# Kernel tuning notes

Hardware: AMD Instinct MI355X
Metric: run time of the kernel (lower is better)

Reference implementation:

```python
import jax, jax.numpy as jnp
import numpy as np

B, N_PER = 1048576, 32
MAX_COUNT = 5  # counts >= 5 lumped into the '>4' bucket (severity 3)


def setup_inputs() -> dict:
    key = jax.random.key(0)
    k1, k2, k3 = jax.random.split(key, 3)
    x1 = jax.random.uniform(k1, (B, N_PER), dtype=jnp.float32)
    x2 = jax.random.uniform(k2, (B, N_PER), dtype=jnp.float32)
    x3 = jax.random.uniform(k3, (B, N_PER), dtype=jnp.float32)
    return {"x1": x1, "x2": x2, "x3": x3}


def _count_distribution(p):
    # p: [B, N] independent fact probabilities.
    # Poisson-binomial DP over facts with count capped at MAX_COUNT (absorbing).
    b = p.shape[0]
    init = jnp.zeros((b, MAX_COUNT + 1), p.dtype).at[:, 0].set(1.0)

    def step(c, pi):
        pi = pi[:, None]                              # [B,1]
        shifted = jnp.pad(c[:, :-1], ((0, 0), (1, 0)))  # count+1
        new = c * (1.0 - pi) + shifted * pi
        # absorbing top bucket: staying in >=MAX_COUNT regardless of pi
        new = new.at[:, -1].add(c[:, -1] * pi[:, 0])
        return new, None

    counts, _ = jax.lax.scan(step, init, p.T)  # scan over facts axis
    return counts  # [B, MAX_COUNT+1]


def reference(x1, x2, x3):
    p = jnp.concatenate([x1, x2, x3], axis=1)  # [B, 96]
    c = _count_distribution(p)
    # severity(0): n==0; severity(1): 1<=n<=2; severity(2): 3<=n<=4;
    # severity(3): n>4; severity(4): never derivable -> 0
    sev = jnp.stack(
        [c[:, 0], c[:, 1] + c[:, 2], c[:, 3] + c[:, 4], c[:, 5],
         jnp.zeros_like(c[:, 0])],
        axis=1,
    )
    return sev  # [B, 5]
```

## Files before the change

kernel.cpp:

```cpp
#include <hip/hip_runtime.h>


#define THREADS 256

__global__ __launch_bounds__(THREADS, 6) void hemorrhage_kernel(
    const float* __restrict__ x1,
    const float* __restrict__ x2,
    const float* __restrict__ x3,
    float* __restrict__ out)
{
    const int t = threadIdx.x;
    const int m = t & 7;
    const int row = blockIdx.x * (THREADS / 8) + (t >> 3);
    const size_t base = (size_t)row * 32 + (size_t)m * 4;

    const float4 p1 = *(const float4*)(x1 + base);
    const float4 p2 = *(const float4*)(x2 + base);
    const float4 p3 = *(const float4*)(x3 + base);

    float a0 = 1.0f, a1 = 0.0f, a2 = 0.0f, a3 = 0.0f, a4 = 0.0f, a5 = 0.0f;

#define STEP(P)                          \
    do {                                 \
        const float p_ = (P);            \
        const float q_ = 1.0f - p_;      \
        a5 = fmaf(a4, p_, a5);           \
        a4 = fmaf(a4, q_, a3 * p_);      \
        a3 = fmaf(a3, q_, a2 * p_);      \
        a2 = fmaf(a2, q_, a1 * p_);      \
        a1 = fmaf(a1, q_, a0 * p_);      \
        a0 = a0 * q_;                    \
    } while (0)

    STEP(p1.x); STEP(p1.y); STEP(p1.z); STEP(p1.w);
    STEP(p2.x); STEP(p2.y); STEP(p2.z); STEP(p2.w);
    STEP(p3.x); STEP(p3.y); STEP(p3.z); STEP(p3.w);
#undef STEP

#pragma unroll
    for (int d = 1; d < 8; d <<= 1) {
        const float b0 = __shfl_xor(a0, d);
        const float b1 = __shfl_xor(a1, d);
        const float b2 = __shfl_xor(a2, d);
        const float b3 = __shfl_xor(a3, d);
        const float b4 = __shfl_xor(a4, d);
        const float b5 = __shfl_xor(a5, d);

        float n0 = a0 * b0;
        float n1 = a0 * b1;
        n1 = fmaf(a1, b0, n1);
        float n2 = a0 * b2;
        n2 = fmaf(a1, b1, n2);
        n2 = fmaf(a2, b0, n2);
        float n3 = a0 * b3;
        n3 = fmaf(a1, b2, n3);
        n3 = fmaf(a2, b1, n3);
        n3 = fmaf(a3, b0, n3);
        float n4 = a0 * b4;
        n4 = fmaf(a1, b3, n4);
        n4 = fmaf(a2, b2, n4);
        n4 = fmaf(a3, b1, n4);
        n4 = fmaf(a4, b0, n4);
        const float n5 = 1.0f - (((n0 + n1) + (n2 + n3)) + n4);

        a0 = n0; a1 = n1; a2 = n2; a3 = n3; a4 = n4; a5 = n5;
    }

    if (m < 5) {
        float v;
        switch (m) {
            case 0: v = a0; break;
            case 1: v = a1 + a2; break;
            case 2: v = a3 + a4; break;
            case 3: v = a5; break;
            default: v = 0.0f; break;
        }
        out[(size_t)row * 5 + m] = v;
    }
}

extern "C" void kernel_launch(void* const* d_in, const int* in_sizes, int n_in,
                              void* d_out, int out_size, void* d_ws, size_t ws_size,
                              hipStream_t stream) {
    const float* x1 = (const float*)d_in[0];
    const float* x2 = (const float*)d_in[1];
    const float* x3 = (const float*)d_in[2];
    float* out = (float*)d_out;

    const int rows = in_sizes[0] / 32;
    const int blocks = rows / (THREADS / 8);
    hemorrhage_kernel<<<blocks, THREADS, 0, stream>>>(x1, x2, x3, out);
}
```

Measured before the change: 346.7 us.

## Process one row per thread with sequential DP instead of shuffle-tree merge

Result: slower. 362.4 us (+4.5%).

```diff
diff --git a/kernel.cpp b/kernel.cpp
--- a/kernel.cpp
+++ b/kernel.cpp
@@ -3,80 +3,55 @@
 
 #define THREADS 256
 
-__global__ __launch_bounds__(THREADS, 6) void hemorrhage_kernel(
+__global__ __launch_bounds__(THREADS, 4) void hemorrhage_kernel(
     const float* __restrict__ x1,
     const float* __restrict__ x2,
     const float* __restrict__ x3,
     float* __restrict__ out)
 {
-    const int t = threadIdx.x;
-    const int m = t & 7;
-    const int row = blockIdx.x * (THREADS / 8) + (t >> 3);
-    const size_t base = (size_t)row * 32 + (size_t)m * 4;
+    const int row = blockIdx.x * THREADS + threadIdx.x;
 
-    const float4 p1 = *(const float4*)(x1 + base);
-    const float4 p2 = *(const float4*)(x2 + base);
-    const float4 p3 = *(const float4*)(x3 + base);
+    const float4* __restrict__ r1 = (const float4*)(x1 + (size_t)row * 32);
+    const float4* __restrict__ r2 = (const float4*)(x2 + (size_t)row * 32);
+    const float4* __restrict__ r3 = (const float4*)(x3 + (size_t)row * 32);
 
-    float a0 = 1.0f, a1 = 0.0f, a2 = 0.0f, a3 = 0.0f, a4 = 0.0f, a5 = 0.0f;
+    float4 v[24];
+#pragma unroll
+    for (int j = 0; j < 8; ++j) v[j] = r1[j];
+#pragma unroll
+    for (int j = 0; j < 8; ++j) v[8 + j] = r2[j];
+#pragma unroll
+    for (int j = 0; j < 8; ++j) v[16 + j] = r3[j];
 
-#define STEP(P)                          \
-    do {                                 \
-        const float p_ = (P);            \
-        const float q_ = 1.0f - p_;      \
-        a5 = fmaf(a4, p_, a5);           \
-        a4 = fmaf(a4, q_, a3 * p_);      \
-        a3 = fmaf(a3, q_, a2 * p_);      \
-        a2 = fmaf(a2, q_, a1 * p_);      \
-        a1 = fmaf(a1, q_, a0 * p_);      \
-        a0 = a0 * q_;                    \
+    float a0 = 1.0f, a1 = 0.0f, a2 = 0.0f, a3 = 0.0f, a4 = 0.0f;
+
+#define STEP(P)                              \
+    do {                                     \
+        const float p_ = (P);                \
+        a4 = fmaf(p_, a3 - a4, a4);          \
+        a3 = fmaf(p_, a2 - a3, a3);          \
+        a2 = fmaf(p_, a1 - a2, a2);          \
+        a1 = fmaf(p_, a0 - a1, a1);          \
+        a0 = fmaf(-p_, a0, a0);              \
     } while (0)
 
-    STEP(p1.x); STEP(p1.y); STEP(p1.z); STEP(p1.w);
-    STEP(p2.x); STEP(p2.y); STEP(p2.z); STEP(p2.w);
-    STEP(p3.x); STEP(p3.y); STEP(p3.z); STEP(p3.w);
+#pragma unroll
+    for (int j = 0; j < 24; ++j) {
+        STEP(v[j].x);
+        STEP(v[j].y);
+        STEP(v[j].z);
+        STEP(v[j].w);
+    }
 #undef STEP
 
-#pragma unroll
-    for (int d = 1; d < 8; d <<= 1) {
-        const float b0 = __shfl_xor(a0, d);
-        const float b1 = __shfl_xor(a1, d);
-        const float b2 = __shfl_xor(a2, d);
-        const float b3 = __shfl_xor(a3, d);
-        const float b4 = __shfl_xor(a4, d);
-        const float b5 = __shfl_xor(a5, d);
+    const float c5 = 1.0f - (((a0 + a1) + (a2 + a3)) + a4);
 
-        float n0 = a0 * b0;
-        float n1 = a0 * b1;
-        n1 = fmaf(a1, b0, n1);
-        float n2 = a0 * b2;
-        n2 = fmaf(a1, b1, n2);
-        n2 = fmaf(a2, b0, n2);
-        float n3 = a0 * b3;
-        n3 = fmaf(a1, b2, n3);
-        n3 = fmaf(a2, b1, n3);
-        n3 = fmaf(a3, b0, n3);
-        float n4 = a0 * b4;
-        n4 = fmaf(a1, b3, n4);
-        n4 = fmaf(a2, b2, n4);
-        n4 = fmaf(a3, b1, n4);
-        n4 = fmaf(a4, b0, n4);
-        const float n5 = 1.0f - (((n0 + n1) + (n2 + n3)) + n4);
-
-        a0 = n0; a1 = n1; a2 = n2; a3 = n3; a4 = n4; a5 = n5;
-    }
-
-    if (m < 5) {
-        float v;
-        switch (m) {
-            case 0: v = a0; break;
-            case 1: v = a1 + a2; break;
-            case 2: v = a3 + a4; break;
-            case 3: v = a5; break;
-            default: v = 0.0f; break;
-        }
-        out[(size_t)row * 5 + m] = v;
-    }
+    float* __restrict__ o = out + (size_t)row * 5;
+    o[0] = a0;
+    o[1] = a1 + a2;
+    o[2] = a3 + a4;
+    o[3] = c5;
+    o[4] = 0.0f;
 }
 
 extern "C" void kernel_launch(void* const* d_in, const int* in_sizes, int n_in,
@@ -88,6 +63,6 @@
     float* out = (float*)d_out;
 
     const int rows = in_sizes[0] / 32;
-    const int blocks = rows / (THREADS / 8);
+    const int blocks = rows / THREADS;
     hemorrhage_kernel<<<blocks, THREADS, 0, stream>>>(x1, x2, x3, out);
 }
```
